# Kernel optimization log

Measured on AMD Instinct MI355X. Metric: run time of the kernel, lower is better.

## Reference

```python
import jax, jax.numpy as jnp
import numpy as np

B, I, H, R = 8192, 512, 1024, 64  # batch, input_size, hidden_size, rank (w_rank == u_ranks[-1])


def setup_inputs() -> dict:
    key = jax.random.key(0)
    ks = jax.random.split(key, 11)
    f = jax.random.normal
    return {
        "x": f(ks[0], (B, I), jnp.float32),
        "h": f(ks[1], (B, H), jnp.float32),
        "c": f(ks[2], (B, H), jnp.float32),
        "u_x": 0.1 * f(ks[3], (I, R), jnp.float32),
        "u_h": 0.1 * f(ks[4], (H, R), jnp.float32),
        "v_x": 0.1 * f(ks[5], (4 * H, R), jnp.float32),
        "v_h": 0.1 * f(ks[6], (4 * H, R), jnp.float32),
        "b_x": 0.1 * f(ks[7], (4 * H,), jnp.float32),
        "b_h": 0.1 * f(ks[8], (4 * H,), jnp.float32),
        "dia_x": 0.1 * f(ks[9], (1, I), jnp.float32),
        "dia_h": 0.1 * f(ks[10], (1, H), jnp.float32),
    }


def reference(x, h, c, u_x, u_h, v_x, v_h, b_x, b_h, dia_x, dia_h):
    Bn = x.shape[0]
    # diagonal (vector-multiplication) terms; vm_x padded to hidden size (H >= I)
    vm_x = jnp.pad(dia_x * x, ((0, 0), (0, H - I)))          # [B, H]
    vm_h = dia_h * h                                          # [B, H]
    # low-rank projections: [B,R] @ [R,4H]
    lowered_x = (x @ u_x) @ v_x.T                             # [B, 4H]
    lowered_h = (h @ u_h) @ v_h.T                             # [B, 4H]
    # vectorized form of the 4-gate refinement loop
    v_x4 = v_x.reshape(4, H, R)
    v_h4 = v_h.reshape(4, H, R)
    coef_x = jnp.sum(u_x[None] * v_x4[:, :I, :], axis=-1)    # [4, I]
    coef_h = jnp.sum(u_h[None] * v_h4, axis=-1)              # [4, H]
    ref_x = jnp.pad(x[:, None, :] * coef_x[None], ((0, 0), (0, 0), (0, H - I))).reshape(Bn, 4 * H)
    ref_h = (h[:, None, :] * coef_h[None]).reshape(Bn, 4 * H)
    gx = lowered_x - ref_x + b_x
    gh = lowered_h - ref_h + b_h
    xi, xf, xo, xn = jnp.split(gx, 4, axis=1)
    hi, hf, ho, hn = jnp.split(gh, 4, axis=1)
    z = vm_x + vm_h
    inputgate = jax.nn.sigmoid(xi + hi + z)
    forgetgate = jax.nn.sigmoid(xf + hf + z)
    outputgate = jax.nn.sigmoid(xo + ho + z)
    newgate = jnp.tanh(xn + hn + z)
    c_next = forgetgate * c + inputgate * newgate
    h_next = outputgate * jnp.tanh(c_next)
    return h_next, c_next
```

## Files before the change

kernel.cpp:

```cpp
#include <hip/hip_runtime.h>
#include <hip/hip_bf16.h>

#define B_ 8192
#define I_ 512
#define H_ 1024
#define R_ 64

typedef __bf16 bf16x8 __attribute__((ext_vector_type(8)));
typedef short  s16x8  __attribute__((ext_vector_type(8)));
typedef float  f32x4  __attribute__((ext_vector_type(4)));

static __device__ __forceinline__ short f2bf(float f) {
    union { float f; unsigned u; } v; v.f = f;
    unsigned r = v.u + 0x7fffu + ((v.u >> 16) & 1u);
    return (short)(r >> 16);
}
static __device__ __forceinline__ float frcp_(float x) {
#if __has_builtin(__builtin_amdgcn_rcpf)
    return __builtin_amdgcn_rcpf(x);
#else
    float r; asm("v_rcp_f32 %0, %1" : "=v"(r) : "v"(x)); return r;
#endif
}
static __device__ __forceinline__ float sigmoidf_(float v) {
    return frcp_(1.f + __expf(-v));
}
static __device__ __forceinline__ float tanhf_(float v) {
    return 2.f * frcp_(1.f + __expf(-2.f * v)) - 1.f;
}

__global__ __launch_bounds__(256) void prep_kernel(
    const float* __restrict__ u_x, const float* __restrict__ u_h,
    const float* __restrict__ v_x, const float* __restrict__ v_h,
    short* __restrict__ uxT, short* __restrict__ uhT, short* __restrict__ Vc,
    float* __restrict__ coef_x, float* __restrict__ coef_h)
{
    int t = blockIdx.x * 256 + threadIdx.x;
    if (t < 64 * 512) {
        int k = t >> 6, r = t & 63;
        uxT[r * 512 + k] = f2bf(u_x[t]);
        return;
    }
    t -= 64 * 512;
    if (t < 64 * 1024) {
        int k = t >> 6, r = t & 63;
        uhT[r * 1024 + k] = f2bf(u_h[t]);
        return;
    }
    t -= 64 * 1024;
    if (t < 4096 * 128) {
        int n = t >> 7, q = t & 127;
        Vc[t] = f2bf(q < 64 ? v_x[n * 64 + q] : v_h[n * 64 + (q - 64)]);
        return;
    }
    t -= 4096 * 128;
    if (t < 1536 * 64) {
        const int wid = t >> 6, lane = t & 63;
        const float* U; const float* V; float* C; int j, JN;
        if (wid < 512) { U = u_x; V = v_x; C = coef_x; j = wid;       JN = 512;  }
        else           { U = u_h; V = v_h; C = coef_h; j = wid - 512; JN = 1024; }
        const float uv = U[(size_t)j * 64 + lane];
        float s[4];
#pragma unroll
        for (int g = 0; g < 4; ++g)
            s[g] = uv * V[(size_t)(g * H_ + j) * 64 + lane];
#pragma unroll
        for (int off = 32; off >= 1; off >>= 1)
#pragma unroll
            for (int g = 0; g < 4; ++g)
                s[g] += __shfl_xor(s[g], off, 64);
        if (lane == 0)
#pragma unroll
            for (int g = 0; g < 4; ++g)
                C[g * JN + j] = s[g];
        return;
    }
}

__global__ __launch_bounds__(256) void stage1_kernel(
    const float* __restrict__ x, const float* __restrict__ h,
    const short* __restrict__ uxT, const short* __restrict__ uhT,
    short* __restrict__ P)
{
    __shared__ short At[16 * 136];
    const int w = threadIdx.x >> 6, lane = threadIdx.x & 63;
    const int quad = lane >> 4, lr = lane & 15;
    const int n0 = w * 16;

    const float* X; const short* UT; int K, co;
    if (blockIdx.y == 0) { X = x; UT = uxT; K = I_; co = 0; }
    else                 { X = h; UT = uhT; K = H_; co = 64; }

    const int b0 = blockIdx.x * 16;
    const int srow = threadIdx.x >> 4;
    const int scol = (threadIdx.x & 15) * 8;

    f32x4 acc = {};
    const short* bp = UT + (size_t)(n0 + lr) * K + quad * 8;
    const short* arow = At + lr * 136 + quad * 8;
    const float* srcbase = X + (size_t)(b0 + srow) * K + scol;

    float4 c0 = ((const float4*)(srcbase))[0];
    float4 c1 = ((const float4*)(srcbase))[1];

    for (int k0 = 0; k0 < K; k0 += 128) {
        s16x8 p;
        p[0] = f2bf(c0.x); p[1] = f2bf(c0.y); p[2] = f2bf(c0.z); p[3] = f2bf(c0.w);
        p[4] = f2bf(c1.x); p[5] = f2bf(c1.y); p[6] = f2bf(c1.z); p[7] = f2bf(c1.w);
        __syncthreads();
        *(s16x8*)(At + srow * 136 + scol) = p;
        __syncthreads();
        if (k0 + 128 < K) {
            c0 = ((const float4*)(srcbase + k0 + 128))[0];
            c1 = ((const float4*)(srcbase + k0 + 128))[1];
        }
#pragma unroll
        for (int ks = 0; ks < 4; ++ks) {
            bf16x8 bfrag = *(const bf16x8*)(bp + k0 + ks * 32);
            bf16x8 afrag = *(const bf16x8*)(arow + ks * 32);
            acc = __builtin_amdgcn_mfma_f32_16x16x32_bf16(afrag, bfrag, acc, 0, 0, 0);
        }
    }

#pragma unroll
    for (int r = 0; r < 4; ++r)
        P[(size_t)(b0 + quad * 4 + r) * 128 + co + n0 + lr] = f2bf(acc[r]);
}

__global__ __launch_bounds__(256) void stage2_kernel(
    const short* __restrict__ P, const short* __restrict__ Vc,
    const float* __restrict__ x, const float* __restrict__ h,
    const float* __restrict__ c,
    const float* __restrict__ coef_x, const float* __restrict__ coef_h,
    const float* __restrict__ b_x, const float* __restrict__ b_h,
    const float* __restrict__ dia_x, const float* __restrict__ dia_h,
    float* __restrict__ out)
{
    const int lane = threadIdx.x & 63;
    const int wv   = threadIdx.x >> 6;
    const int quad = lane >> 4, lr = lane & 15;
    const int b0 = blockIdx.x * 64;
    const int j0 = blockIdx.y * 64 + wv * 16;
    const int j4 = j0 + quad * 4;
    const bool jx = (j0 < I_);

    bf16x8 a[4];
#pragma unroll
    for (int ks = 0; ks < 4; ++ks)
        a[ks] = *(const bf16x8*)(P + (size_t)(b0 + lr) * 128 + ks * 32 + quad * 8);
    f32x4 xv = {}, hv, cv;
    {
        const int brow = b0 + lr;
        cv = *(const f32x4*)(c + (size_t)brow * H_ + j4);
        hv = *(const f32x4*)(h + (size_t)brow * H_ + j4);
        if (jx) xv = *(const f32x4*)(x + (size_t)brow * I_ + j4);
    }

    bf16x8 vfr[4][4];
#pragma unroll
    for (int g = 0; g < 4; ++g)
#pragma unroll
        for (int ks = 0; ks < 4; ++ks)
            vfr[g][ks] = *(const bf16x8*)(Vc + (size_t)(g * H_ + j0 + lr) * 128 + ks * 32 + quad * 8);

    float dx[4] = {}, dh[4], cx[4][4] = {}, ch[4][4], bs[4][4];
    {
        f32x4 t;
        if (jx) { t = *(const f32x4*)(dia_x + j4); dx[0]=t[0]; dx[1]=t[1]; dx[2]=t[2]; dx[3]=t[3]; }
        t = *(const f32x4*)(dia_h + j4); dh[0]=t[0]; dh[1]=t[1]; dh[2]=t[2]; dh[3]=t[3];
#pragma unroll
        for (int g = 0; g < 4; ++g) {
            if (jx) {
                t = *(const f32x4*)(coef_x + g * I_ + j4);
                cx[g][0]=t[0]; cx[g][1]=t[1]; cx[g][2]=t[2]; cx[g][3]=t[3];
            }
            t = *(const f32x4*)(coef_h + g * H_ + j4);
            ch[g][0]=t[0]; ch[g][1]=t[1]; ch[g][2]=t[2]; ch[g][3]=t[3];
            f32x4 tb = *(const f32x4*)(b_x + g * H_ + j4);
            f32x4 th = *(const f32x4*)(b_h + g * H_ + j4);
            bs[g][0]=tb[0]+th[0]; bs[g][1]=tb[1]+th[1]; bs[g][2]=tb[2]+th[2]; bs[g][3]=tb[3]+th[3];
        }
    }

    for (int mt = 0; mt < 4; ++mt) {
        bf16x8 an[4];
        f32x4 xn = {}, hn, cn2;
        if (mt < 3) {
            const int rb = b0 + (mt + 1) * 16 + lr;
#pragma unroll
            for (int ks = 0; ks < 4; ++ks)
                an[ks] = *(const bf16x8*)(P + (size_t)rb * 128 + ks * 32 + quad * 8);
            cn2 = *(const f32x4*)(c + (size_t)rb * H_ + j4);
            hn  = *(const f32x4*)(h + (size_t)rb * H_ + j4);
            if (jx) xn = *(const f32x4*)(x + (size_t)rb * I_ + j4);
        }

        f32x4 acc[4] = {};
#pragma unroll
        for (int ks = 0; ks < 4; ++ks)
#pragma unroll
            for (int g = 0; g < 4; ++g)
                acc[g] = __builtin_amdgcn_mfma_f32_16x16x32_bf16(vfr[g][ks], a[ks], acc[g], 0, 0, 0);

        {
            const int brow = b0 + mt * 16 + lr;
            float hw[4], cw[4];
#pragma unroll
            for (int r = 0; r < 4; ++r) {
                const float xe = xv[r], he = hv[r];
                const float z  = dx[r] * xe + dh[r] * he;

                const float g0 = acc[0][r] - xe * cx[0][r] - he * ch[0][r] + bs[0][r] + z;
                const float g1 = acc[1][r] - xe * cx[1][r] - he * ch[1][r] + bs[1][r] + z;
                const float g2 = acc[2][r] - xe * cx[2][r] - he * ch[2][r] + bs[2][r] + z;
                const float g3 = acc[3][r] - xe * cx[3][r] - he * ch[3][r] + bs[3][r] + z;

                const float ig = sigmoidf_(g0);
                const float fg = sigmoidf_(g1);
                const float og = sigmoidf_(g2);
                const float ng = tanhf_(g3);

                cw[r] = fg * cv[r] + ig * ng;
                hw[r] = og * tanhf_(cw[r]);
            }
            f32x4 hq = { hw[0], hw[1], hw[2], hw[3] };
            f32x4 cq = { cw[0], cw[1], cw[2], cw[3] };
            __builtin_nontemporal_store(hq, (f32x4*)(out + (size_t)brow * H_ + j4));
            __builtin_nontemporal_store(cq, (f32x4*)(out + (size_t)B_ * H_ + (size_t)brow * H_ + j4));
        }

        if (mt < 3) {
#pragma unroll
            for (int ks = 0; ks < 4; ++ks) a[ks] = an[ks];
            xv = xn; hv = hn; cv = cn2;
        }
    }
}

extern "C" void kernel_launch(void* const* d_in, const int* in_sizes, int n_in,
                              void* d_out, int out_size, void* d_ws, size_t ws_size,
                              hipStream_t stream) {
    const float* x     = (const float*)d_in[0];
    const float* h     = (const float*)d_in[1];
    const float* c     = (const float*)d_in[2];
    const float* u_x   = (const float*)d_in[3];
    const float* u_h   = (const float*)d_in[4];
    const float* v_x   = (const float*)d_in[5];
    const float* v_h   = (const float*)d_in[6];
    const float* b_x   = (const float*)d_in[7];
    const float* b_h   = (const float*)d_in[8];
    const float* dia_x = (const float*)d_in[9];
    const float* dia_h = (const float*)d_in[10];
    float* out = (float*)d_out;

    char* ws = (char*)d_ws;
    short* P      = (short*)(ws);
    short* uxT    = (short*)(ws + 2097152);
    short* uhT    = (short*)(ws + 2097152 + 65536);
    short* Vc     = (short*)(ws + 2097152 + 65536 + 131072);
    float* coef_x = (float*)(ws + 2097152 + 65536 + 131072 + 1048576);
    float* coef_h = (float*)(ws + 2097152 + 65536 + 131072 + 1048576 + 8192);

    prep_kernel<<<2816, 256, 0, stream>>>(u_x, u_h, v_x, v_h, uxT, uhT, Vc, coef_x, coef_h);
    stage1_kernel<<<dim3(512, 2), 256, 0, stream>>>(x, h, uxT, uhT, P);
    stage2_kernel<<<dim3(128, 16), 256, 0, stream>>>(P, Vc, x, h, c,
                                                     coef_x, coef_h, b_x, b_h,
                                                     dia_x, dia_h, out);
}
```

Baseline: 213.2 us.

## Restructure stage2 to row-stationary tiles and fold diagonal, coef and bias terms

Stage2 now keeps one 16-row P fragment per wave and sweeps 256 hidden columns, reloading V fragments per column tile instead of reusing V across batch rows. The launch changes to 256 blocks of 512 threads. The prep kernel pre-combines dia minus coef into AX/AH and pre-sums the two biases, which cuts per-element arithmetic and parameter loads. The outputs switch from nontemporal to plain stores. The cost is 64 V fragment loads per column tile with no batch reuse, and a grid of only 256 blocks.

```diff
diff --git a/kernel.cpp b/kernel.cpp
--- a/kernel.cpp
+++ b/kernel.cpp
@@ -32,8 +32,10 @@
 __global__ __launch_bounds__(256) void prep_kernel(
     const float* __restrict__ u_x, const float* __restrict__ u_h,
     const float* __restrict__ v_x, const float* __restrict__ v_h,
+    const float* __restrict__ b_x, const float* __restrict__ b_h,
+    const float* __restrict__ dia_x, const float* __restrict__ dia_h,
     short* __restrict__ uxT, short* __restrict__ uhT, short* __restrict__ Vc,
-    float* __restrict__ coef_x, float* __restrict__ coef_h)
+    float* __restrict__ AX, float* __restrict__ AH, float* __restrict__ BS)
 {
     int t = blockIdx.x * 256 + threadIdx.x;
     if (t < 64 * 512) {
@@ -56,9 +58,10 @@
     t -= 4096 * 128;
     if (t < 1536 * 64) {
         const int wid = t >> 6, lane = t & 63;
-        const float* U; const float* V; float* C; int j, JN;
-        if (wid < 512) { U = u_x; V = v_x; C = coef_x; j = wid;       JN = 512;  }
-        else           { U = u_h; V = v_h; C = coef_h; j = wid - 512; JN = 1024; }
+        const float* U; const float* V; int j;
+        const bool isx = (wid < 512);
+        if (isx) { U = u_x; V = v_x; j = wid;       }
+        else     { U = u_h; V = v_h; j = wid - 512; }
         const float uv = U[(size_t)j * 64 + lane];
         float s[4];
 #pragma unroll
@@ -69,10 +72,20 @@
 #pragma unroll
             for (int g = 0; g < 4; ++g)
                 s[g] += __shfl_xor(s[g], off, 64);
-        if (lane == 0)
-#pragma unroll
-            for (int g = 0; g < 4; ++g)
-                C[g * JN + j] = s[g];
+        if (lane == 0) {
+            if (isx) {
+#pragma unroll
+                for (int g = 0; g < 4; ++g)
+                    AX[g * 1024 + j] = dia_x[j] - s[g];
+            } else {
+#pragma unroll
+                for (int g = 0; g < 4; ++g) {
+                    AH[g * 1024 + j] = dia_h[j] - s[g];
+                    BS[g * 1024 + j] = b_x[g * H_ + j] + b_h[g * H_ + j];
+                    if (j >= 512) AX[g * 1024 + j] = 0.f;
+                }
+            }
+        }
         return;
     }
 }
@@ -127,72 +140,60 @@
         P[(size_t)(b0 + quad * 4 + r) * 128 + co + n0 + lr] = f2bf(acc[r]);
 }
 
-__global__ __launch_bounds__(256) void stage2_kernel(
+__global__ __launch_bounds__(512) void stage2_kernel(
     const short* __restrict__ P, const short* __restrict__ Vc,
     const float* __restrict__ x, const float* __restrict__ h,
     const float* __restrict__ c,
-    const float* __restrict__ coef_x, const float* __restrict__ coef_h,
-    const float* __restrict__ b_x, const float* __restrict__ b_h,
-    const float* __restrict__ dia_x, const float* __restrict__ dia_h,
+    const float* __restrict__ AX, const float* __restrict__ AH,
+    const float* __restrict__ BS,
     float* __restrict__ out)
 {
-    const int lane = threadIdx.x & 63;
-    const int wv   = threadIdx.x >> 6;
+    const int tid  = threadIdx.x;
+    const int lane = tid & 63, wv = tid >> 6;
     const int quad = lane >> 4, lr = lane & 15;
-    const int b0 = blockIdx.x * 64;
-    const int j0 = blockIdx.y * 64 + wv * 16;
-    const int j4 = j0 + quad * 4;
-    const bool jx = (j0 < I_);
+    const int rowg = wv >> 2, jg = wv & 3;
+    const int row  = blockIdx.x * 32 + rowg * 16 + lr;
+    const int jbase = jg * 256;
+    const bool jx = (jg < 2);
 
     bf16x8 a[4];
 #pragma unroll
     for (int ks = 0; ks < 4; ++ks)
-        a[ks] = *(const bf16x8*)(P + (size_t)(b0 + lr) * 128 + ks * 32 + quad * 8);
+        a[ks] = *(const bf16x8*)(P + (size_t)row * 128 + ks * 32 + quad * 8);
+
     f32x4 xv = {}, hv, cv;
     {
-        const int brow = b0 + lr;
-        cv = *(const f32x4*)(c + (size_t)brow * H_ + j4);
-        hv = *(const f32x4*)(h + (size_t)brow * H_ + j4);
-        if (jx) xv = *(const f32x4*)(x + (size_t)brow * I_ + j4);
-    }
-
-    bf16x8 vfr[4][4];
-#pragma unroll
-    for (int g = 0; g < 4; ++g)
-#pragma unroll
-        for (int ks = 0; ks < 4; ++ks)
-            vfr[g][ks] = *(const bf16x8*)(Vc + (size_t)(g * H_ + j0 + lr) * 128 + ks * 32 + quad * 8);
-
-    float dx[4] = {}, dh[4], cx[4][4] = {}, ch[4][4], bs[4][4];
-    {
-        f32x4 t;
-        if (jx) { t = *(const f32x4*)(dia_x + j4); dx[0]=t[0]; dx[1]=t[1]; dx[2]=t[2]; dx[3]=t[3]; }
-        t = *(const f32x4*)(dia_h + j4); dh[0]=t[0]; dh[1]=t[1]; dh[2]=t[2]; dh[3]=t[3];
+        const int j4 = jbase + quad * 4;
+        cv = *(const f32x4*)(c + (size_t)row * H_ + j4);
+        hv = *(const f32x4*)(h + (size_t)row * H_ + j4);
+        if (jx) xv = *(const f32x4*)(x + (size_t)row * I_ + j4);
+    }
+
+    for (int t = 0; t < 16; ++t) {
+        const int jt = jbase + t * 16;
+        const int j4 = jt + quad * 4;
+
+        bf16x8 vfr[4][4];
+#pragma unroll
+        for (int g = 0; g < 4; ++g)
+#pragma unroll
+            for (int ks = 0; ks < 4; ++ks)
+                vfr[g][ks] = *(const bf16x8*)(Vc + (size_t)(g * H_ + jt + lr) * 128 + ks * 32 + quad * 8);
+
+        f32x4 ax[4] = {}, ah[4], bs[4];
 #pragma unroll
         for (int g = 0; g < 4; ++g) {
-            if (jx) {
-                t = *(const f32x4*)(coef_x + g * I_ + j4);
-                cx[g][0]=t[0]; cx[g][1]=t[1]; cx[g][2]=t[2]; cx[g][3]=t[3];
-            }
-            t = *(const f32x4*)(coef_h + g * H_ + j4);
-            ch[g][0]=t[0]; ch[g][1]=t[1]; ch[g][2]=t[2]; ch[g][3]=t[3];
-            f32x4 tb = *(const f32x4*)(b_x + g * H_ + j4);
-            f32x4 th = *(const f32x4*)(b_h + g * H_ + j4);
-            bs[g][0]=tb[0]+th[0]; bs[g][1]=tb[1]+th[1]; bs[g][2]=tb[2]+th[2]; bs[g][3]=tb[3]+th[3];
-        }
-    }
-
-    for (int mt = 0; mt < 4; ++mt) {
-        bf16x8 an[4];
-        f32x4 xn = {}, hn, cn2;
-        if (mt < 3) {
-            const int rb = b0 + (mt + 1) * 16 + lr;
-#pragma unroll
-            for (int ks = 0; ks < 4; ++ks)
-                an[ks] = *(const bf16x8*)(P + (size_t)rb * 128 + ks * 32 + quad * 8);
-            cn2 = *(const f32x4*)(c + (size_t)rb * H_ + j4);
-            hn  = *(const f32x4*)(h + (size_t)rb * H_ + j4);
-            if (jx) xn = *(const f32x4*)(x + (size_t)rb * I_ + j4);
+            if (jx) ax[g] = *(const f32x4*)(AX + g * 1024 + j4);
+            ah[g] = *(const f32x4*)(AH + g * 1024 + j4);
+            bs[g] = *(const f32x4*)(BS + g * 1024 + j4);
+        }
+
+        f32x4 xn = {}, hn, cn;
+        if (t < 15) {
+            const int jn = j4 + 16;
+            cn = *(const f32x4*)(c + (size_t)row * H_ + jn);
+            hn = *(const f32x4*)(h + (size_t)row * H_ + jn);
+            if (jx) xn = *(const f32x4*)(x + (size_t)row * I_ + jn);
         }
 
         f32x4 acc[4] = {};
@@ -202,38 +203,30 @@
             for (int g = 0; g < 4; ++g)
                 acc[g] = __builtin_amdgcn_mfma_f32_16x16x32_bf16(vfr[g][ks], a[ks], acc[g], 0, 0, 0);
 
-        {
-            const int brow = b0 + mt * 16 + lr;
-            float hw[4], cw[4];
-#pragma unroll
-            for (int r = 0; r < 4; ++r) {
-                const float xe = xv[r], he = hv[r];
-                const float z  = dx[r] * xe + dh[r] * he;
-
-                const float g0 = acc[0][r] - xe * cx[0][r] - he * ch[0][r] + bs[0][r] + z;
-                const float g1 = acc[1][r] - xe * cx[1][r] - he * ch[1][r] + bs[1][r] + z;
-                const float g2 = acc[2][r] - xe * cx[2][r] - he * ch[2][r] + bs[2][r] + z;
-                const float g3 = acc[3][r] - xe * cx[3][r] - he * ch[3][r] + bs[3][r] + z;
-
-                const float ig = sigmoidf_(g0);
-                const float fg = sigmoidf_(g1);
-                const float og = sigmoidf_(g2);
-                const float ng = tanhf_(g3);
-
-                cw[r] = fg * cv[r] + ig * ng;
-                hw[r] = og * tanhf_(cw[r]);
-            }
-            f32x4 hq = { hw[0], hw[1], hw[2], hw[3] };
-            f32x4 cq = { cw[0], cw[1], cw[2], cw[3] };
-            __builtin_nontemporal_store(hq, (f32x4*)(out + (size_t)brow * H_ + j4));
-            __builtin_nontemporal_store(cq, (f32x4*)(out + (size_t)B_ * H_ + (size_t)brow * H_ + j4));
-        }
-
-        if (mt < 3) {
-#pragma unroll
-            for (int ks = 0; ks < 4; ++ks) a[ks] = an[ks];
-            xv = xn; hv = hn; cv = cn2;
-        }
+        float hw[4], cw[4];
+#pragma unroll
+        for (int r = 0; r < 4; ++r) {
+            const float xe = xv[r], he = hv[r];
+
+            const float g0 = acc[0][r] + xe * ax[0][r] + he * ah[0][r] + bs[0][r];
+            const float g1 = acc[1][r] + xe * ax[1][r] + he * ah[1][r] + bs[1][r];
+            const float g2 = acc[2][r] + xe * ax[2][r] + he * ah[2][r] + bs[2][r];
+            const float g3 = acc[3][r] + xe * ax[3][r] + he * ah[3][r] + bs[3][r];
+
+            const float ig = sigmoidf_(g0);
+            const float fg = sigmoidf_(g1);
+            const float og = sigmoidf_(g2);
+            const float ng = tanhf_(g3);
+
+            cw[r] = fg * cv[r] + ig * ng;
+            hw[r] = og * tanhf_(cw[r]);
+        }
+        f32x4 hq = { hw[0], hw[1], hw[2], hw[3] };
+        f32x4 cq = { cw[0], cw[1], cw[2], cw[3] };
+        *(f32x4*)(out + (size_t)row * H_ + j4) = hq;
+        *(f32x4*)(out + (size_t)B_ * H_ + (size_t)row * H_ + j4) = cq;
+
+        xv = xn; hv = hn; cv = cn;
     }
 }
 
@@ -254,16 +247,16 @@
     float* out = (float*)d_out;
 
     char* ws = (char*)d_ws;
-    short* P      = (short*)(ws);
-    short* uxT    = (short*)(ws + 2097152);
-    short* uhT    = (short*)(ws + 2097152 + 65536);
-    short* Vc     = (short*)(ws + 2097152 + 65536 + 131072);
-    float* coef_x = (float*)(ws + 2097152 + 65536 + 131072 + 1048576);
-    float* coef_h = (float*)(ws + 2097152 + 65536 + 131072 + 1048576 + 8192);
-
-    prep_kernel<<<2816, 256, 0, stream>>>(u_x, u_h, v_x, v_h, uxT, uhT, Vc, coef_x, coef_h);
+    short* P   = (short*)(ws);
+    short* uxT = (short*)(ws + 2097152);
+    short* uhT = (short*)(ws + 2097152 + 65536);
+    short* Vc  = (short*)(ws + 2097152 + 65536 + 131072);
+    float* AX  = (float*)(ws + 2097152 + 65536 + 131072 + 1048576);
+    float* AH  = (float*)(ws + 2097152 + 65536 + 131072 + 1048576 + 16384);
+    float* BS  = (float*)(ws + 2097152 + 65536 + 131072 + 1048576 + 32768);
+
+    prep_kernel<<<2816, 256, 0, stream>>>(u_x, u_h, v_x, v_h, b_x, b_h, dia_x, dia_h,
+                                          uxT, uhT, Vc, AX, AH, BS);
     stage1_kernel<<<dim3(512, 2), 256, 0, stream>>>(x, h, uxT, uhT, P);
-    stage2_kernel<<<dim3(128, 16), 256, 0, stream>>>(P, Vc, x, h, c,
-                                                     coef_x, coef_h, b_x, b_h,
-                                                     dia_x, dia_h, out);
-}
+    stage2_kernel<<<256, 512, 0, stream>>>(P, Vc, x, h, c, AX, AH, BS, out);
+}
```

After: 235.4 us. 10.4% more time.
